# Optimization experiments

Measured on AMD Instinct MI355X. Metric: run time of the kernel, lower is better.

The kernel has to match this reference:

```python
import jax, jax.numpy as jnp
import numpy as np

# Config: B=16, channels C=16, feature_num D=4, node_num K=128, L=128, emb E=10
# c_in for the 1x1 conv = (order*support_len + 1) * C = (2*3 + 1)*16 = 112

def setup_inputs() -> dict:
    key = jax.random.key(0)
    ks = jax.random.split(key, 8)
    B, C, D, K, L, E = 16, 16, 4, 128, 128, 10
    return {
        "x": jax.random.normal(ks[0], (B, C, D * K * L), dtype=jnp.float32),
        "supports": jax.random.uniform(ks[1], (2, K, K), dtype=jnp.float32),
        "nodevec1": jax.random.normal(ks[2], (D, K, E), dtype=jnp.float32),
        "nodevec2": jax.random.normal(ks[3], (D, E, K), dtype=jnp.float32),
        "imp_W": jax.random.normal(ks[4], (K, K), dtype=jnp.float32) * 0.05,
        "imp_b": jax.random.normal(ks[5], (K,), dtype=jnp.float32) * 0.05,
        "mlp_W": jax.random.normal(ks[6], (D, C, 7 * C), dtype=jnp.float32) * 0.05,
        "mlp_b": jax.random.normal(ks[7], (D, C), dtype=jnp.float32) * 0.05,
        "B": B, "C": C, "D": D, "K": K, "L": L,
    }


def reference(x, supports, nodevec1, nodevec2, imp_W, imp_b, mlp_W, mlp_b, B, C, D, K, L):
    # x: (B, C, D*K*L) -> (D, B*L, C, K)  [matches reshape/permute in torch forward]
    xr = x.reshape(B, C, D, K, L).transpose(2, 0, 4, 1, 3).reshape(D, B * L, C, K)

    # adaptive adjacency per feature
    # torch: importance = Linear(nv1.T).T  => imp[j,e] = sum_k W[j,k] nv1[k,e] + b[j]
    imp = jnp.einsum('jk,fke->fje', imp_W, nodevec1) + imp_b[None, :, None]
    nv1m = nodevec1 * imp                                   # (D, K, E)
    scores = jnp.einsum('fke,fej->fkj', nv1m, nodevec2)     # (D, K, K)
    adp = jax.nn.softmax(jax.nn.relu(scores), axis=2)       # softmax over dim=1 of (K,K)

    # multi-hop diffusion: out[n,c,w] = sum_v x[n,c,v] * a[w,v], order=2
    outs = [xr]
    for s in range(2):  # two shared supports
        a = supports[s]
        x1 = jnp.einsum('fncv,wv->fncw', xr, a)
        x2 = jnp.einsum('fncv,wv->fncw', x1, a)
        outs.append(x1)
        outs.append(x2)
    x1 = jnp.einsum('fncv,fwv->fncw', xr, adp)  # per-feature adaptive support
    x2 = jnp.einsum('fncv,fwv->fncw', x1, adp)
    outs.append(x1)
    outs.append(x2)

    cat = jnp.concatenate(outs, axis=2)  # (D, B*L, 7C, K)

    # per-feature 1x1 conv = channel GEMM
    y = jnp.einsum('fnck,foc->fnok', cat, mlp_W) + mlp_b[:, None, :, None]  # (D, N, C, K)

    y = y.reshape(D, B, L, C, K)
    y = jnp.transpose(y, (1, 2, 0, 3, 4))  # (B, L, D, C, K) == torch.stack(res, dim=2)
    y = jnp.transpose(y, (0, 3, 2, 4, 1))  # (B, C, D, K, L)
    return y.reshape(B, C, D * K * L)
```

## Files before the change

kernel.cpp:

```cpp
#include <hip/hip_runtime.h>


namespace {

constexpr int Kn = 128;
constexpr int En = 10;

typedef __attribute__((ext_vector_type(8))) short short8;
typedef __attribute__((ext_vector_type(4))) float f32x4;

__device__ inline unsigned short f2bf(float f) {
    unsigned x = __float_as_uint(f);
    return (unsigned short)((x + 0x7FFFu + ((x >> 16) & 1u)) >> 16);
}
__device__ inline unsigned pack2(float lo, float hi) {
    return (unsigned)f2bf(lo) | ((unsigned)f2bf(hi) << 16);
}

__global__ __launch_bounds__(256) void build_adj(
    const float* __restrict__ supports,
    const float* __restrict__ nv1,
    const float* __restrict__ nv2,
    const float* __restrict__ impW,
    const float* __restrict__ impB,
    float* __restrict__ mats)
{
    const int tid = threadIdx.x;
    const int blk = blockIdx.x;
    if (blk < 2) {
        const float* A = supports + blk * Kn * Kn;
        float* dst = mats + (blk * 2) * Kn * Kn;
        for (int i = tid; i < Kn * Kn; i += 256) dst[i] = A[i];
        return;
    }
    const int d = blk - 2;
    __shared__ float nv1m[Kn * En];
    __shared__ float nv2s[En * Kn];
    for (int i = tid; i < Kn * En; i += 256) nv1m[i] = nv1[d * Kn * En + i];
    for (int i = tid; i < En * Kn; i += 256) nv2s[i] = nv2[d * En * Kn + i];
    __syncthreads();
    float impv[5];
    #pragma unroll
    for (int r = 0; r < 5; ++r) {
        const int idx = tid + r * 256;
        const int j = idx / En, e = idx - j * En;
        float acc = impB[j];
        for (int kk = 0; kk < Kn; ++kk)
            acc += impW[j * Kn + kk] * nv1m[kk * En + e];
        impv[r] = acc;
    }
    __syncthreads();
    #pragma unroll
    for (int r = 0; r < 5; ++r) nv1m[tid + r * 256] *= impv[r];
    __syncthreads();
    if (tid < Kn) {
        const int k = tid;
        float a[En];
        #pragma unroll
        for (int e = 0; e < En; ++e) a[e] = nv1m[k * En + e];
        float mx = 0.f;
        for (int j = 0; j < Kn; ++j) {
            float s = 0.f;
            #pragma unroll
            for (int e = 0; e < En; ++e) s += a[e] * nv2s[e * Kn + j];
            mx = fmaxf(mx, s);
        }
        float sum = 0.f;
        for (int j = 0; j < Kn; ++j) {
            float s = 0.f;
            #pragma unroll
            for (int e = 0; e < En; ++e) s += a[e] * nv2s[e * Kn + j];
            s = fmaxf(s, 0.f);
            sum += expf(s - mx);
        }
        const float inv = 1.f / sum;
        float* dst = mats + (4 + d) * Kn * Kn;
        for (int j = 0; j < Kn; ++j) {
            float s = 0.f;
            #pragma unroll
            for (int e = 0; e < En; ++e) s += a[e] * nv2s[e * Kn + j];
            s = fmaxf(s, 0.f);
            dst[k * Kn + j] = expf(s - mx) * inv;
        }
    }
}

__global__ __launch_bounds__(256) void square_cvt(
    const float* __restrict__ fm, unsigned short* __restrict__ wbm)
{
    const int tid = threadIdx.x;
    if (blockIdx.x < 96) {
        __shared__ float S[Kn * Kn];
        const int m = blockIdx.x >> 4, strip = blockIdx.x & 15;
        const int src = (m == 0) ? 0 : (m == 1) ? 2 : (2 + m);
        const int dst = (m == 0) ? 2 : (m == 1) ? 4 : (2 + 2 * m);
        const float* s = fm + src * Kn * Kn;
        unsigned short* o = wbm + dst * Kn * Kn;
        for (int i = tid; i < Kn * Kn; i += 256) S[i] = s[i];
        __syncthreads();
        const int v = strip * 8 + (tid >> 5);
        const int k0 = (tid & 31) * 4;
        float acc0 = 0.f, acc1 = 0.f, acc2 = 0.f, acc3 = 0.f;
        for (int u0 = 0; u0 < Kn; u0 += 4) {
            const float4 av = *reinterpret_cast<const float4*>(&S[v * Kn + u0]);
            const float a[4] = {av.x, av.y, av.z, av.w};
            #pragma unroll
            for (int j = 0; j < 4; ++j) {
                const float4 m4 = *reinterpret_cast<const float4*>(&S[(u0 + j) * Kn + k0]);
                acc0 += a[j] * m4.x; acc1 += a[j] * m4.y;
                acc2 += a[j] * m4.z; acc3 += a[j] * m4.w;
            }
        }
        uint2 r;
        r.x = pack2(acc0, acc1);
        r.y = pack2(acc2, acc3);
        *reinterpret_cast<uint2*>(&o[v * Kn + k0]) = r;
    } else {
        const int s = blockIdx.x - 96;
        const int wslot = (s == 0) ? 0 : (s == 1) ? 1 : (s == 2) ? 3 : (5 + 2 * (s - 3));
        const int fsrc  = (s == 0) ? -1 : (s == 1) ? 0 : (s == 2) ? 2 : (4 + (s - 3));
        for (int i = tid; i < Kn * Kn; i += 256) {
            const int k = i >> 7, v = i & 127;
            const float val = (fsrc < 0) ? ((k == v) ? 1.f : 0.f) : fm[fsrc * 16384 + i];
            wbm[wslot * 16384 + i] = f2bf(val);
        }
    }
}

__global__ __launch_bounds__(256, 2) void fused_mfma(
    const float* __restrict__ x,
    const unsigned short* __restrict__ wbm,
    const float* __restrict__ mlpW,
    const float* __restrict__ mlpB,
    float* __restrict__ out)
{
    __shared__ __align__(16) char lds[32768];
    const int tid = threadIdx.x;
    const int lane = tid & 63, lr = lane & 15, lg = lane >> 4;
    const int wid = tid >> 6, wr = wid >> 1, wk = wid & 1;

    const unsigned u = blockIdx.x;
    const unsigned pid = (u & 7) * 256 + (u >> 3);
    const int kh = pid & 1;
    const int lt = (pid >> 1) & 15;
    const int b  = (pid >> 5) & 15;
    const int d  = (int)(pid >> 9);
    const int l0 = lt * 8;

    const f32x4 zero4 = {0.f, 0.f, 0.f, 0.f};
    short8 Mb0[8], Mb1[8];
    const unsigned short* mbase = wbm + kh * 8192 + wk * 4096 + lr * 128 + lg * 8;

    auto loadM = [&](int slot, short8 (&dst)[8]) {
        const unsigned short* mp = mbase + slot * 16384;
        #pragma unroll
        for (int j = 0; j < 2; ++j)
            #pragma unroll
            for (int ks = 0; ks < 4; ++ks)
                dst[j * 4 + ks] =
                    *reinterpret_cast<const short8*>(mp + j * 2048 + ks * 32);
    };

    loadM(0, Mb0);

    {
        const int half = tid & 1;
        const int p5 = (tid >> 1) & 31;
        #pragma unroll
        for (int i = 0; i < 8; ++i) {
            const int g = i * 4 + wid;
            const int c = g >> 1, pg = g & 1;
            const int p = pg * 32 + p5;
            const int v = p * 2;
            const float* p0 = x + (size_t)b * 1048576 + c * 65536 + d * 16384 +
                              v * 128 + l0 + half * 4;
            const float4 q0 = *reinterpret_cast<const float4*>(p0);
            const float4 q1 = *reinterpret_cast<const float4*>(p0 + 128);
            const float a0[4] = {q0.x, q0.y, q0.z, q0.w};
            const float a1[4] = {q1.x, q1.y, q1.z, q1.w};
            const int colb = (4 * p) ^ ((c & 7) << 4);
            #pragma unroll
            for (int j = 0; j < 4; ++j) {
                const int n = half * 4 + j;
                *reinterpret_cast<unsigned*>(lds + (n * 16 + c) * 256 + colb) =
                    pack2(a0[j], a1[j]);
            }
        }
    }

    short8 Wf[4];
    #pragma unroll
    for (int p = 0; p < 4; ++p) {
        short8 w;
        #pragma unroll
        for (int j = 0; j < 8; ++j) {
            const int tc = lg * 8 + j, t = 2 * p + (tc >> 4), c = tc & 15;
            const float wv = (t < 7) ? mlpW[d * 1792 + lr * 112 + t * 16 + c] : 0.f;
            w[j] = (short)f2bf(wv);
        }
        Wf[p] = w;
    }

    __syncthreads();

    short8 Xf[4][4];
    {
        const int swz = (lr & 7) << 4;
        #pragma unroll
        for (int rti = 0; rti < 4; ++rti) {
            const int base = ((wr * 4 + rti) * 16 + lr) * 256;
            #pragma unroll
            for (int ks = 0; ks < 4; ++ks)
                Xf[rti][ks] = *reinterpret_cast<const short8*>(
                    lds + base + ((ks * 64 + lg * 16) ^ swz));
        }
    }
    __syncthreads();

    f32x4 Y[2][4];
    #pragma unroll
    for (int ni = 0; ni < 2; ++ni)
        #pragma unroll
        for (int kt = 0; kt < 4; ++kt) Y[ni][kt] = zero4;

    auto phaseA_Z = [&](const short8 (&cur)[8], int tp, bool zeroTail) {
        f32x4 D[4][2];
        #pragma unroll
        for (int rti = 0; rti < 4; ++rti) { D[rti][0] = zero4; D[rti][1] = zero4; }
        #pragma unroll
        for (int ks = 0; ks < 4; ++ks) {
            #pragma unroll
            for (int rti = 0; rti < 4; ++rti) {
                D[rti][0] = __builtin_amdgcn_mfma_f32_16x16x32_bf16(
                    Xf[rti][ks], cur[ks], D[rti][0], 0, 0, 0);
                D[rti][1] = __builtin_amdgcn_mfma_f32_16x16x32_bf16(
                    Xf[rti][ks], cur[4 + ks], D[rti][1], 0, 0, 0);
            }
        }
        #pragma unroll
        for (int rti = 0; rti < 4; ++rti) {
            #pragma unroll
            for (int j = 0; j < 2; ++j) {
                const int n = wr * 4 + rti;
                const int kp = (wk * 2 + j) * 16 + lr;
                uint2 zz;
                zz.x = pack2(D[rti][j][0], D[rti][j][1]);
                zz.y = pack2(D[rti][j][2], D[rti][j][3]);
                *reinterpret_cast<uint2*>(
                    lds + n * 4096 + ((kp * 64 + tp * 32 + lg * 8) ^ ((kp & 7) << 4))) = zz;
                if (zeroTail) {
                    const uint2 z0 = {0u, 0u};
                    *reinterpret_cast<uint2*>(
                        lds + n * 4096 + ((kp * 64 + 32 + lg * 8) ^ ((kp & 7) << 4))) = z0;
                }
            }
        }
    };

    auto phaseB = [&](const short8& Wfp) {
        #pragma unroll
        for (int ni = 0; ni < 2; ++ni) {
            const int n = wid * 2 + ni;
            #pragma unroll
            for (int ktl = 0; ktl < 4; ++ktl) {
                const int kp = ktl * 16 + lr;
                const short8 Bfz = *reinterpret_cast<const short8*>(
                    lds + n * 4096 + ((kp * 64 + lg * 16) ^ ((kp & 7) << 4)));
                Y[ni][ktl] = __builtin_amdgcn_mfma_f32_16x16x32_bf16(
                    Wfp, Bfz, Y[ni][ktl], 0, 0, 0);
            }
        }
    };

    loadM(1, Mb1);              phaseA_Z(Mb0, 0, false);
    loadM(2, Mb0);              phaseA_Z(Mb1, 1, false);
    __syncthreads();  phaseB(Wf[0]);  __syncthreads();
    loadM(3, Mb1);              phaseA_Z(Mb0, 0, false);
    loadM(4, Mb0);              phaseA_Z(Mb1, 1, false);
    __syncthreads();  phaseB(Wf[1]);  __syncthreads();
    loadM(5 + 2 * d, Mb1);      phaseA_Z(Mb0, 0, false);
    loadM(6 + 2 * d, Mb0);      phaseA_Z(Mb1, 1, false);
    __syncthreads();  phaseB(Wf[2]);  __syncthreads();
                                phaseA_Z(Mb0, 0, true);
    __syncthreads();  phaseB(Wf[3]);  __syncthreads();

    #pragma unroll
    for (int ni = 0; ni < 2; ++ni) {
        const int l = wid * 2 + ni;
        #pragma unroll
        for (int ktl = 0; ktl < 4; ++ktl) {
            const int k = ktl * 16 + lr;
            #pragma unroll
            for (int r = 0; r < 4; ++r) {
                const int o = lg * 4 + r;
                *reinterpret_cast<float*>(
                    lds + o * 2048 + k * 32 + ((l * 4) ^ (k & 12))) = Y[ni][ktl][r];
            }
        }
    }
    __syncthreads();

    {
        const int half = tid & 1;
        const int klo = (tid >> 1) & 31;
        #pragma unroll
        for (int i = 0; i < 8; ++i) {
            const int g = i * 4 + wid;
            const int o = g >> 1, kg = g & 1;
            const int k = kg * 32 + klo;
            const int pp = (k >> 2) & 3;
            const float4 F = *reinterpret_cast<const float4*>(
                lds + o * 2048 + k * 32 + half * 16);
            float4 s1, s2;
            if (pp & 1) { s1.x = F.y; s1.y = F.x; s1.z = F.w; s1.w = F.z; }
            else        { s1 = F; }
            if (pp & 2) { s2.x = s1.z; s2.y = s1.w; s2.z = s1.x; s2.w = s1.y; }
            else        { s2 = s1; }
            const float bv = mlpB[d * 16 + o];
            s2.x += bv; s2.y += bv; s2.z += bv; s2.w += bv;
            float* gp = out + (size_t)b * 1048576 + o * 65536 + d * 16384 +
                        (kh * 64 + k) * 128 + l0 + half * 4;
            *reinterpret_cast<float4*>(gp) = s2;
        }
    }
}

}

extern "C" void kernel_launch(void* const* d_in, const int* in_sizes, int n_in,
                              void* d_out, int out_size, void* d_ws, size_t ws_size,
                              hipStream_t stream)
{
    const float* x    = (const float*)d_in[0];
    const float* sup  = (const float*)d_in[1];
    const float* nv1  = (const float*)d_in[2];
    const float* nv2  = (const float*)d_in[3];
    const float* impW = (const float*)d_in[4];
    const float* impB = (const float*)d_in[5];
    const float* mlpW = (const float*)d_in[6];
    const float* mlpB = (const float*)d_in[7];
    float* outp = (float*)d_out;

    float* fm = (float*)d_ws;
    unsigned short* wbm = (unsigned short*)((char*)d_ws + 786432);

    build_adj<<<6, 256, 0, stream>>>(sup, nv1, nv2, impW, impB, fm);
    square_cvt<<<103, 256, 0, stream>>>(fm, wbm);
    fused_mfma<<<2048, 256, 0, stream>>>(x, wbm, mlpW, mlpB, outp);
}
```

Baseline: 140.2 us.

## Halve l-tile per block and give each wave private Z scratch to drop barriers

Each block now handles 4 l-positions instead of 8, doubling the grid to 4096 blocks. Each wave owns a 16-row slice of the output k dimension and its own LDS region for the intermediate Z tiles. This removes the __syncthreads between phase A and phase B. The M fragments are triple-buffered in registers to prefetch further ahead. In exchange, each block re-reads the adjacency matrices for fewer l-columns, which doubles global M traffic, and x loads become 4-wide scalar bf16 stores into LDS.

```diff
diff --git a/kernel.cpp b/kernel.cpp
--- a/kernel.cpp
+++ b/kernel.cpp
@@ -137,55 +137,38 @@
     __shared__ __align__(16) char lds[32768];
     const int tid = threadIdx.x;
     const int lane = tid & 63, lr = lane & 15, lg = lane >> 4;
-    const int wid = tid >> 6, wr = wid >> 1, wk = wid & 1;
+    const int wid = tid >> 6;
 
     const unsigned u = blockIdx.x;
-    const unsigned pid = (u & 7) * 256 + (u >> 3);
+    const unsigned pid = (u & 7) * 512 + (u >> 3);
     const int kh = pid & 1;
-    const int lt = (pid >> 1) & 15;
-    const int b  = (pid >> 5) & 15;
-    const int d  = (int)(pid >> 9);
-    const int l0 = lt * 8;
-
-    const f32x4 zero4 = {0.f, 0.f, 0.f, 0.f};
-    short8 Mb0[8], Mb1[8];
-    const unsigned short* mbase = wbm + kh * 8192 + wk * 4096 + lr * 128 + lg * 8;
-
-    auto loadM = [&](int slot, short8 (&dst)[8]) {
+    const int lt = (pid >> 1) & 31;
+    const int b  = (pid >> 6) & 15;
+    const int d  = (int)(pid >> 10);
+    const int l0 = lt * 4;
+
+    const unsigned short* mbase = wbm + (kh * 64 + wid * 16 + lr) * 128 + lg * 8;
+    short8 Ma[4], Mb_[4], Mc[4];
+    auto loadM = [&](int slot, short8 (&dst)[4]) {
         const unsigned short* mp = mbase + slot * 16384;
         #pragma unroll
-        for (int j = 0; j < 2; ++j)
-            #pragma unroll
-            for (int ks = 0; ks < 4; ++ks)
-                dst[j * 4 + ks] =
-                    *reinterpret_cast<const short8*>(mp + j * 2048 + ks * 32);
+        for (int ks = 0; ks < 4; ++ks)
+            dst[ks] = *reinterpret_cast<const short8*>(mp + ks * 32);
     };
-
-    loadM(0, Mb0);
-
-    {
-        const int half = tid & 1;
-        const int p5 = (tid >> 1) & 31;
-        #pragma unroll
-        for (int i = 0; i < 8; ++i) {
-            const int g = i * 4 + wid;
-            const int c = g >> 1, pg = g & 1;
-            const int p = pg * 32 + p5;
-            const int v = p * 2;
-            const float* p0 = x + (size_t)b * 1048576 + c * 65536 + d * 16384 +
-                              v * 128 + l0 + half * 4;
-            const float4 q0 = *reinterpret_cast<const float4*>(p0);
-            const float4 q1 = *reinterpret_cast<const float4*>(p0 + 128);
-            const float a0[4] = {q0.x, q0.y, q0.z, q0.w};
-            const float a1[4] = {q1.x, q1.y, q1.z, q1.w};
-            const int colb = (4 * p) ^ ((c & 7) << 4);
-            #pragma unroll
-            for (int j = 0; j < 4; ++j) {
-                const int n = half * 4 + j;
-                *reinterpret_cast<unsigned*>(lds + (n * 16 + c) * 256 + colb) =
-                    pack2(a0[j], a1[j]);
-            }
-        }
+    loadM(0, Ma); loadM(1, Mb_); loadM(2, Mc);
+
+    #pragma unroll
+    for (int it = 0; it < 8; ++it) {
+        const int idx = it * 256 + tid;
+        const int v = idx & 127, c = idx >> 7;
+        const float* gp = x + (size_t)b * 1048576 + c * 65536 + d * 16384 + v * 128 + l0;
+        const float4 q = *reinterpret_cast<const float4*>(gp);
+        const float qa[4] = {q.x, q.y, q.z, q.w};
+        const int colb = (2 * v) ^ ((c & 7) << 4);
+        #pragma unroll
+        for (int n = 0; n < 4; ++n)
+            *reinterpret_cast<unsigned short*>(lds + (n * 16 + c) * 256 + colb) =
+                f2bf(qa[n]);
     }
 
     short8 Wf[4];
@@ -207,121 +190,99 @@
     {
         const int swz = (lr & 7) << 4;
         #pragma unroll
-        for (int rti = 0; rti < 4; ++rti) {
-            const int base = ((wr * 4 + rti) * 16 + lr) * 256;
+        for (int n = 0; n < 4; ++n) {
+            const int base = (n * 16 + lr) * 256;
             #pragma unroll
             for (int ks = 0; ks < 4; ++ks)
-                Xf[rti][ks] = *reinterpret_cast<const short8*>(
+                Xf[n][ks] = *reinterpret_cast<const short8*>(
                     lds + base + ((ks * 64 + lg * 16) ^ swz));
         }
     }
     __syncthreads();
 
-    f32x4 Y[2][4];
-    #pragma unroll
-    for (int ni = 0; ni < 2; ++ni)
-        #pragma unroll
-        for (int kt = 0; kt < 4; ++kt) Y[ni][kt] = zero4;
-
-    auto phaseA_Z = [&](const short8 (&cur)[8], int tp, bool zeroTail) {
-        f32x4 D[4][2];
-        #pragma unroll
-        for (int rti = 0; rti < 4; ++rti) { D[rti][0] = zero4; D[rti][1] = zero4; }
-        #pragma unroll
-        for (int ks = 0; ks < 4; ++ks) {
-            #pragma unroll
-            for (int rti = 0; rti < 4; ++rti) {
-                D[rti][0] = __builtin_amdgcn_mfma_f32_16x16x32_bf16(
-                    Xf[rti][ks], cur[ks], D[rti][0], 0, 0, 0);
-                D[rti][1] = __builtin_amdgcn_mfma_f32_16x16x32_bf16(
-                    Xf[rti][ks], cur[4 + ks], D[rti][1], 0, 0, 0);
+    const f32x4 zero4 = {0.f, 0.f, 0.f, 0.f};
+    char* zb = lds + 16384 + wid * 4096;
+
+    f32x4 Yacc[4];
+    #pragma unroll
+    for (int n = 0; n < 4; ++n) Yacc[n] = zero4;
+
+    auto phaseA = [&](const short8 (&cur)[4], int tp, bool zeroTail) {
+        f32x4 D[4];
+        #pragma unroll
+        for (int n = 0; n < 4; ++n) D[n] = zero4;
+        #pragma unroll
+        for (int ks = 0; ks < 4; ++ks)
+            #pragma unroll
+            for (int n = 0; n < 4; ++n)
+                D[n] = __builtin_amdgcn_mfma_f32_16x16x32_bf16(
+                    Xf[n][ks], cur[ks], D[n], 0, 0, 0);
+        #pragma unroll
+        for (int n = 0; n < 4; ++n) {
+            uint2 zz;
+            zz.x = pack2(D[n][0], D[n][1]);
+            zz.y = pack2(D[n][2], D[n][3]);
+            *reinterpret_cast<uint2*>(
+                zb + n * 1024 + lr * 64 + ((tp * 32 + lg * 8) ^ ((lr & 3) << 4))) = zz;
+            if (zeroTail) {
+                const uint2 z0 = {0u, 0u};
+                *reinterpret_cast<uint2*>(
+                    zb + n * 1024 + lr * 64 + ((32 + lg * 8) ^ ((lr & 3) << 4))) = z0;
             }
         }
-        #pragma unroll
-        for (int rti = 0; rti < 4; ++rti) {
-            #pragma unroll
-            for (int j = 0; j < 2; ++j) {
-                const int n = wr * 4 + rti;
-                const int kp = (wk * 2 + j) * 16 + lr;
-                uint2 zz;
-                zz.x = pack2(D[rti][j][0], D[rti][j][1]);
-                zz.y = pack2(D[rti][j][2], D[rti][j][3]);
-                *reinterpret_cast<uint2*>(
-                    lds + n * 4096 + ((kp * 64 + tp * 32 + lg * 8) ^ ((kp & 7) << 4))) = zz;
-                if (zeroTail) {
-                    const uint2 z0 = {0u, 0u};
-                    *reinterpret_cast<uint2*>(
-                        lds + n * 4096 + ((kp * 64 + 32 + lg * 8) ^ ((kp & 7) << 4))) = z0;
-                }
-            }
-        }
     };
-
     auto phaseB = [&](const short8& Wfp) {
         #pragma unroll
-        for (int ni = 0; ni < 2; ++ni) {
-            const int n = wid * 2 + ni;
-            #pragma unroll
-            for (int ktl = 0; ktl < 4; ++ktl) {
-                const int kp = ktl * 16 + lr;
-                const short8 Bfz = *reinterpret_cast<const short8*>(
-                    lds + n * 4096 + ((kp * 64 + lg * 16) ^ ((kp & 7) << 4)));
-                Y[ni][ktl] = __builtin_amdgcn_mfma_f32_16x16x32_bf16(
-                    Wfp, Bfz, Y[ni][ktl], 0, 0, 0);
-            }
+        for (int n = 0; n < 4; ++n) {
+            const short8 Bfz = *reinterpret_cast<const short8*>(
+                zb + n * 1024 + lr * 64 + ((lg * 16) ^ ((lr & 3) << 4)));
+            Yacc[n] = __builtin_amdgcn_mfma_f32_16x16x32_bf16(
+                Wfp, Bfz, Yacc[n], 0, 0, 0);
         }
     };
 
-    loadM(1, Mb1);              phaseA_Z(Mb0, 0, false);
-    loadM(2, Mb0);              phaseA_Z(Mb1, 1, false);
-    __syncthreads();  phaseB(Wf[0]);  __syncthreads();
-    loadM(3, Mb1);              phaseA_Z(Mb0, 0, false);
-    loadM(4, Mb0);              phaseA_Z(Mb1, 1, false);
-    __syncthreads();  phaseB(Wf[1]);  __syncthreads();
-    loadM(5 + 2 * d, Mb1);      phaseA_Z(Mb0, 0, false);
-    loadM(6 + 2 * d, Mb0);      phaseA_Z(Mb1, 1, false);
-    __syncthreads();  phaseB(Wf[2]);  __syncthreads();
-                                phaseA_Z(Mb0, 0, true);
-    __syncthreads();  phaseB(Wf[3]);  __syncthreads();
-
-    #pragma unroll
-    for (int ni = 0; ni < 2; ++ni) {
-        const int l = wid * 2 + ni;
-        #pragma unroll
-        for (int ktl = 0; ktl < 4; ++ktl) {
-            const int k = ktl * 16 + lr;
+    phaseA(Ma, 0, false);  loadM(3, Ma);
+    phaseA(Mb_, 1, false); loadM(4, Mb_);
+    phaseB(Wf[0]);
+    phaseA(Mc, 0, false);  loadM(5 + 2 * d, Mc);
+    phaseA(Ma, 1, false);  loadM(6 + 2 * d, Ma);
+    phaseB(Wf[1]);
+    phaseA(Mb_, 0, false);
+    phaseA(Mc, 1, false);
+    phaseB(Wf[2]);
+    phaseA(Ma, 0, true);
+    phaseB(Wf[3]);
+
+    {
+        const int kp64 = wid * 16 + lr;
+        #pragma unroll
+        for (int n = 0; n < 4; ++n) {
             #pragma unroll
             for (int r = 0; r < 4; ++r) {
                 const int o = lg * 4 + r;
                 *reinterpret_cast<float*>(
-                    lds + o * 2048 + k * 32 + ((l * 4) ^ (k & 12))) = Y[ni][ktl][r];
+                    lds + o * 1024 + kp64 * 16 + ((n * 4) ^ (kp64 & 12))) = Yacc[n][r];
             }
         }
     }
     __syncthreads();
 
-    {
-        const int half = tid & 1;
-        const int klo = (tid >> 1) & 31;
-        #pragma unroll
-        for (int i = 0; i < 8; ++i) {
-            const int g = i * 4 + wid;
-            const int o = g >> 1, kg = g & 1;
-            const int k = kg * 32 + klo;
-            const int pp = (k >> 2) & 3;
-            const float4 F = *reinterpret_cast<const float4*>(
-                lds + o * 2048 + k * 32 + half * 16);
-            float4 s1, s2;
-            if (pp & 1) { s1.x = F.y; s1.y = F.x; s1.z = F.w; s1.w = F.z; }
-            else        { s1 = F; }
-            if (pp & 2) { s2.x = s1.z; s2.y = s1.w; s2.z = s1.x; s2.w = s1.y; }
-            else        { s2 = s1; }
-            const float bv = mlpB[d * 16 + o];
-            s2.x += bv; s2.y += bv; s2.z += bv; s2.w += bv;
-            float* gp = out + (size_t)b * 1048576 + o * 65536 + d * 16384 +
-                        (kh * 64 + k) * 128 + l0 + half * 4;
-            *reinterpret_cast<float4*>(gp) = s2;
-        }
+    #pragma unroll
+    for (int i = 0; i < 4; ++i) {
+        const int o = i * 4 + wid;
+        const int kp64 = lane;
+        const int pp = (kp64 >> 2) & 3;
+        const float4 F = *reinterpret_cast<const float4*>(lds + o * 1024 + kp64 * 16);
+        float4 s1, s2;
+        if (pp & 1) { s1.x = F.y; s1.y = F.x; s1.z = F.w; s1.w = F.z; }
+        else        { s1 = F; }
+        if (pp & 2) { s2.x = s1.z; s2.y = s1.w; s2.z = s1.x; s2.w = s1.y; }
+        else        { s2 = s1; }
+        const float bv = mlpB[d * 16 + o];
+        s2.x += bv; s2.y += bv; s2.z += bv; s2.w += bv;
+        float* gp = out + (size_t)b * 1048576 + o * 65536 + d * 16384 +
+                    (kh * 64 + kp64) * 128 + l0;
+        *reinterpret_cast<float4*>(gp) = s2;
     }
 }
 
@@ -346,5 +307,5 @@
 
     build_adj<<<6, 256, 0, stream>>>(sup, nv1, nv2, impW, impB, fm);
     square_cvt<<<103, 256, 0, stream>>>(fm, wbm);
-    fused_mfma<<<2048, 256, 0, stream>>>(x, wbm, mlpW, mlpB, outp);
-}
+    fused_mfma<<<4096, 256, 0, stream>>>(x, wbm, mlpW, mlpB, outp);
+}
```

Result: slower. 168.3 us (+20.0%).
